# Kernel optimization log

Measured on AMD Instinct MI355X. Metric: run time of the kernel, lower is better.

Reference implementation:

```python
import jax, jax.numpy as jnp
import numpy as np

N_DISEASE, N_GENE, E, D = 20000, 100000, 2000000, 128


def setup_inputs() -> dict:
    key = jax.random.key(0)
    ks = jax.random.split(key, 12)
    s = 0.05  # weight scale keeps exp(logstd) well-behaved
    return {
        "x_disease": jax.random.normal(ks[0], (N_DISEASE, D), jnp.float32),
        "x_gene": jax.random.normal(ks[1], (N_GENE, D), jnp.float32),
        "edge_src": jax.random.randint(ks[2], (E,), 0, N_DISEASE, jnp.int32),
        "edge_dst": jax.random.randint(ks[3], (E,), 0, N_GENE, jnp.int32),
        "eps": jax.random.normal(ks[4], (N_GENE, D), jnp.float32),
        # SAGEConv (disease->gene): lin_l (on aggregated neighbors, with bias), lin_r (on dst root, no bias)
        "W_l": jax.random.normal(ks[5], (D, D), jnp.float32) * s,
        "b_l": jnp.zeros((D,), jnp.float32),
        "W_r": jax.random.normal(ks[6], (D, D), jnp.float32) * s,
        # fc_mu_gene / fc_logvar_gene
        "mu_W": jax.random.normal(ks[7], (D, D), jnp.float32) * s,
        "mu_b": jnp.zeros((D,), jnp.float32),
        "lv_W": jax.random.normal(ks[8], (D, D), jnp.float32) * s,
        "lv_b": jnp.zeros((D,), jnp.float32),
    }


def reference(x_disease, x_gene, edge_src, edge_dst, eps,
              W_l, b_l, W_r, mu_W, mu_b, lv_W, lv_b):
    # --- SAGEConv('disease' -> 'gene'), aggr='mean' ---
    msg = x_disease[edge_src]                                   # [E, D] gather
    summed = jax.ops.segment_sum(msg, edge_dst, num_segments=N_GENE)   # [N_gene, D]
    cnt = jax.ops.segment_sum(jnp.ones((msg.shape[0],), msg.dtype), edge_dst,
                              num_segments=N_GENE)
    mean = summed / jnp.maximum(cnt, 1.0)[:, None]
    h_gene = mean @ W_l + b_l + x_gene @ W_r                    # [N_gene, D]
    # (HeteroConv aggr='mean' is identity: only one relation targets 'gene')

    # --- mu / logstd heads + VGAE reparametrize ---
    mu = h_gene @ mu_W + mu_b
    logstd = h_gene @ lv_W + lv_b
    z = mu + eps * jnp.exp(logstd)
    return z
```

## Files before the change

### kernel.cpp

```cpp
#include <hip/hip_runtime.h>
#include <math.h>

#define D 128
#define ST 64
#define GBIN 256
#define CAP 6144
#define BCAP 8192
#define BK2_E 16
#define NBMAX 512

typedef short bf16x8 __attribute__((ext_vector_type(8)));
typedef short bf16x4 __attribute__((ext_vector_type(4)));
typedef float f32x4 __attribute__((ext_vector_type(4)));
typedef float f32x2 __attribute__((ext_vector_type(2)));

#if __has_builtin(__builtin_amdgcn_cvt_pk_f32_fp8) && __has_builtin(__builtin_amdgcn_cvt_pk_fp8_f32)
#define HW_FP8 1
#else
#define HW_FP8 0
#endif

__device__ inline unsigned short f2bf(float f) {
    union { float f; unsigned u; } v; v.f = f;
    unsigned r = v.u + 0x7fff + ((v.u >> 16) & 1);
    return (unsigned short)(r >> 16);
}
__device__ inline float bf2f(unsigned short u) {
    union { unsigned u; float f; } v; v.u = ((unsigned)u) << 16;
    return v.f;
}

__device__ inline unsigned f2fp8(float f) {
    union { float f; unsigned u; } v; v.f = f;
    unsigned s = v.u >> 31;
    unsigned mag = v.u & 0x7fffffffu;
    if (mag > 0x43E00000u) mag = 0x43E00000u;
    unsigned r = mag + 0x7FFFFu + ((mag >> 20) & 1);
    int e = (int)(r >> 23) - 120;
    unsigned out;
    if (e <= 0) {
        float ax;
        { union { unsigned u; float f; } w; w.u = mag; ax = w.f; }
        int m = (int)(ax * 512.0f + 0.5f);
        out = (m > 7) ? 8u : (unsigned)m;
    } else {
        out = ((unsigned)e << 3) | ((r >> 20) & 7);
    }
    return (s << 7) | out;
}
__device__ inline float fp8dec(unsigned b) {
    unsigned s = b >> 7, em = b & 0x7f;
    union { unsigned u; float f; } w;
    w.u = (em << 20) + 0x3C000000u;
    float v = (em >= 8) ? w.f : (float)(int)em * 0.001953125f;
    return s ? -v : v;
}

__device__ inline unsigned pack_fp8x4(float4 a) {
#if HW_FP8
    int r = __builtin_amdgcn_cvt_pk_fp8_f32(a.x, a.y, 0, false);
    r = __builtin_amdgcn_cvt_pk_fp8_f32(a.z, a.w, r, true);
    return (unsigned)r;
#else
    return f2fp8(a.x) | (f2fp8(a.y) << 8) | (f2fp8(a.z) << 16) | (f2fp8(a.w) << 24);
#endif
}
__device__ inline void unpack_fp8x4_add(unsigned w, f32x2* acc01, f32x2* acc23) {
#if HW_FP8
    f32x2 p0 = __builtin_amdgcn_cvt_pk_f32_fp8(w, false);
    f32x2 p1 = __builtin_amdgcn_cvt_pk_f32_fp8(w, true);
    *acc01 += p0;
    *acc23 += p1;
#else
    f32x2 p0 = { fp8dec(w & 0xff), fp8dec((w >> 8) & 0xff) };
    f32x2 p1 = { fp8dec((w >> 16) & 0xff), fp8dec((w >> 24) & 0xff) };
    *acc01 += p0;
    *acc23 += p1;
#endif
}

__global__ void init_bcur_kernel(int* __restrict__ bcur, int nbin)
{
    int b = blockIdx.x * blockDim.x + threadIdx.x;
    if (b < nbin) bcur[b] = b * BCAP;
}

__global__ __launch_bounds__(256) void bucket2_kernel(
    const int* __restrict__ esrc, const int* __restrict__ edst,
    int* __restrict__ bcur, unsigned* __restrict__ pairs2, int E, int nbin)
{
    __shared__ int lcount[NBMAX];
    __shared__ int lbase[NBMAX];
    int t = threadIdx.x;
    const int batch = 256 * BK2_E;
    for (long long base = (long long)blockIdx.x * batch; base < E;
         base += (long long)gridDim.x * batch) {
        for (int b = t; b < nbin; b += 256) lcount[b] = 0;
        __syncthreads();
        int bb[BK2_E], rr[BK2_E];
        unsigned pv[BK2_E];
        #pragma unroll
        for (int j = 0; j < BK2_E; ++j) {
            int e = (int)base + t + j * 256;
            bb[j] = -1;
            if (e < E) {
                int dd = __builtin_nontemporal_load(&edst[e]);
                int ss = __builtin_nontemporal_load(&esrc[e]);
                int bin = dd >> 8;
                bb[j] = bin;
                pv[j] = ((unsigned)(dd & (GBIN - 1)) << 16) | (unsigned)ss;
                rr[j] = atomicAdd(&lcount[bin], 1);
            }
        }
        __syncthreads();
        for (int b = t; b < nbin; b += 256)
            lbase[b] = lcount[b] ? atomicAdd(&bcur[b], lcount[b]) : 0;
        __syncthreads();
        #pragma unroll
        for (int j = 0; j < BK2_E; ++j)
            if (bb[j] >= 0) {
                int pos = lbase[bb[j]] + rr[j];
                if (pos < (bb[j] + 1) * BCAP)
                    pairs2[pos] = pv[j];
            }
        __syncthreads();
    }
}

__global__ __launch_bounds__(256) void fill3b_kernel(
    const unsigned* __restrict__ pairs2, const int* __restrict__ bcur,
    int* __restrict__ offs, int* __restrict__ oend,
    unsigned short* __restrict__ csr, int ngene)
{
    __shared__ int lhist[GBIN];
    __shared__ int lofs[GBIN];
    __shared__ int lcur[GBIN];
    __shared__ unsigned short stage[CAP];
    int b = blockIdx.x;
    int t = threadIdx.x;
    int g0 = b * GBIN;
    int ng = min(GBIN, ngene - g0);
    int sb = b * BCAP;
    int se = min(bcur[b], sb + BCAP);
    int n = se - sb;

    lhist[t] = 0;
    __syncthreads();
    for (int i = sb + t; i < se; i += 256)
        atomicAdd(&lhist[pairs2[i] >> 16], 1);
    __syncthreads();
    int v = lhist[t];
    lofs[t] = v;
    __syncthreads();
    for (int off = 1; off < GBIN; off <<= 1) {
        int add = (t >= off) ? lofs[t - off] : 0;
        __syncthreads();
        lofs[t] += add;
        __syncthreads();
    }
    int myofs = lofs[t] - v;
    lcur[t] = myofs;
    if (t < ng) {
        offs[g0 + t] = sb + myofs;
        oend[g0 + t] = sb + myofs + v;
    }
    __syncthreads();

    if (n <= CAP) {
        for (int i = sb + t; i < se; i += 256) {
            unsigned u = pairs2[i];
            int pos = atomicAdd(&lcur[u >> 16], 1);
            stage[pos] = (unsigned short)(u & 0xffffu);
        }
        __syncthreads();
        for (int i = t; i < n; i += 256)
            csr[sb + i] = stage[i];
    } else {
        for (int i = sb + t; i < se; i += 256) {
            unsigned u = pairs2[i];
            int pos = atomicAdd(&lcur[u >> 16], 1);
            csr[sb + pos] = (unsigned short)(u & 0xffffu);
        }
    }
}

__global__ __launch_bounds__(256) void cvt_kernel(
    const float* __restrict__ xd, unsigned char* __restrict__ xdb8, int nxd,
    const float* __restrict__ w0, const float* __restrict__ w1,
    const float* __restrict__ w2, const float* __restrict__ w3,
    unsigned short* __restrict__ t0, unsigned short* __restrict__ t1,
    unsigned short* __restrict__ t2, unsigned short* __restrict__ t3)
{
    int b = blockIdx.x;
    if (b < nxd) {
        int i = b * 256 + threadIdx.x;
        float4 a = ((const float4*)xd)[i * 2];
        float4 c = ((const float4*)xd)[i * 2 + 1];
        ((uint2*)xdb8)[i] = make_uint2(pack_fp8x4(a), pack_fp8x4(c));
    } else {
        int m = b - nxd;
        const float* src = m == 0 ? w0 : m == 1 ? w1 : m == 2 ? w2 : w3;
        unsigned short* dst = m == 0 ? t0 : m == 1 ? t1 : m == 2 ? t2 : t3;
        for (int idx = threadIdx.x; idx < D * D; idx += 256) {
            int k = idx >> 7, n = idx & 127;
            dst[n * D + k] = f2bf(src[idx]);
        }
    }
}

__global__ __launch_bounds__(256, 6) void gather_kernel(
    const int* __restrict__ offs, const int* __restrict__ oend,
    const unsigned short* __restrict__ csr,
    const unsigned char* __restrict__ xdb8, unsigned short* __restrict__ meanb,
    int ngene)
{
    int tid = threadIdx.x;
    int r = tid >> 4, c = tid & 15;
    int row = blockIdx.x * 16 + r;
    if (row >= ngene) return;
    int beg = offs[row], end = oend[row];
    const uint2* tab = (const uint2*)xdb8;
    f32x2 a0[4] = {{0,0},{0,0},{0,0},{0,0}};
    f32x2 a1[4] = {{0,0},{0,0},{0,0},{0,0}};
    int i = beg;
    for (; i + 2 <= end; i += 2) {
        int s0 = csr[i], s1 = csr[i + 1];
        uint2 v0 = tab[s0 * 16 + c];
        uint2 v1 = tab[s1 * 16 + c];
        unpack_fp8x4_add(v0.x, &a0[0], &a0[1]);
        unpack_fp8x4_add(v0.y, &a0[2], &a0[3]);
        unpack_fp8x4_add(v1.x, &a1[0], &a1[1]);
        unpack_fp8x4_add(v1.y, &a1[2], &a1[3]);
    }
    if (i < end) {
        int s0 = csr[i];
        uint2 v0 = tab[s0 * 16 + c];
        unpack_fp8x4_add(v0.x, &a0[0], &a0[1]);
        unpack_fp8x4_add(v0.y, &a0[2], &a0[3]);
    }
    float inv = 1.0f / fmaxf((float)(end - beg), 1.0f);
    bf16x8 o;
    #pragma unroll
    for (int j = 0; j < 4; ++j) {
        f32x2 s = a0[j] + a1[j];
        o[j * 2]     = (short)f2bf(s[0] * inv);
        o[j * 2 + 1] = (short)f2bf(s[1] * inv);
    }
    ((bf16x8*)meanb)[row * 16 + c] = o;
}

__global__ __launch_bounds__(512, 4) void hz_kernel(
    const unsigned short* __restrict__ meanb, const float* __restrict__ xg,
    const float* __restrict__ eps,
    const unsigned short* __restrict__ WlT, const unsigned short* __restrict__ WrT,
    const unsigned short* __restrict__ muT, const unsigned short* __restrict__ lvT,
    const float* __restrict__ bl, const float* __restrict__ mub,
    const float* __restrict__ lvb, float* __restrict__ z, int ngene, int nst)
{
    __shared__ unsigned short mean_s[ST][132];
    __shared__ unsigned short xg_s[ST][132];
    __shared__ unsigned short h_s[ST][132];

    int tid = threadIdx.x;
    int wave = tid >> 6;
    int lane = tid & 63;
    int lr = lane & 15;
    int lg = lane >> 4;
    int cb = wave * 16;
    int nb = cb + lg * 4;

    float4 bl4 = *(const float4*)&bl[nb];
    float4 mb4 = *(const float4*)&mub[nb];
    float4 lb4 = *(const float4*)&lvb[nb];

    for (int st = blockIdx.x; st < nst; st += gridDim.x) {
        int rowbase = st * ST;

        f32x4 epr[4];
        #pragma unroll
        for (int rt = 0; rt < 4; ++rt) {
            int orow = rowbase + rt * 16 + lr;
            if (orow >= ngene) orow = ngene - 1;
            epr[rt] = *(const f32x4*)&eps[(size_t)orow * D + nb];
        }

        for (int i = tid; i < ST * 16; i += 512) {
            int row = i >> 4, c = i & 15;
            int grow = rowbase + row;
            if (grow >= ngene) grow = ngene - 1;
            *(bf16x8*)&mean_s[row][c * 8] =
                *(const bf16x8*)&meanb[(size_t)grow * D + c * 8];
            const float* xp = &xg[(size_t)grow * D + c * 8];
            float4 x0 = *(const float4*)xp;
            float4 x1 = *(const float4*)(xp + 4);
            bf16x8 v;
            v[0] = (short)f2bf(x0.x); v[1] = (short)f2bf(x0.y);
            v[2] = (short)f2bf(x0.z); v[3] = (short)f2bf(x0.w);
            v[4] = (short)f2bf(x1.x); v[5] = (short)f2bf(x1.y);
            v[6] = (short)f2bf(x1.z); v[7] = (short)f2bf(x1.w);
            *(bf16x8*)&xg_s[row][c * 8] = v;
        }
        __syncthreads();

        {
            bf16x8 wl[4], wr[4];
            #pragma unroll
            for (int kc = 0; kc < 4; ++kc) {
                int koff = kc * 32 + lg * 8;
                wl[kc] = *(const bf16x8*)&WlT[(cb + lr) * D + koff];
                wr[kc] = *(const bf16x8*)&WrT[(cb + lr) * D + koff];
            }
            #pragma unroll
            for (int rt = 0; rt < 4; ++rt) {
                int r0 = rt * 16 + lr;
                f32x4 accm = {bl4.x, bl4.y, bl4.z, bl4.w};
                f32x4 accx = {0.f, 0.f, 0.f, 0.f};
                #pragma unroll
                for (int kc = 0; kc < 4; ++kc) {
                    int koff = kc * 32 + lg * 8;
                    bf16x8 am = *(const bf16x8*)&mean_s[r0][koff];
                    bf16x8 ax = *(const bf16x8*)&xg_s[r0][koff];
                    accm = __builtin_amdgcn_mfma_f32_16x16x32_bf16(wl[kc], am, accm, 0, 0, 0);
                    accx = __builtin_amdgcn_mfma_f32_16x16x32_bf16(wr[kc], ax, accx, 0, 0, 0);
                }
                bf16x4 hp;
                #pragma unroll
                for (int r = 0; r < 4; ++r) hp[r] = (short)f2bf(accm[r] + accx[r]);
                *(bf16x4*)&h_s[r0][nb] = hp;
            }
        }
        __syncthreads();

        {
            bf16x8 mu[4], lv[4];
            #pragma unroll
            for (int kc = 0; kc < 4; ++kc) {
                int koff = kc * 32 + lg * 8;
                mu[kc] = *(const bf16x8*)&muT[(cb + lr) * D + koff];
                lv[kc] = *(const bf16x8*)&lvT[(cb + lr) * D + koff];
            }
            #pragma unroll
            for (int rt = 0; rt < 4; ++rt) {
                int r0 = rt * 16 + lr;
                f32x4 zm = {mb4.x, mb4.y, mb4.z, mb4.w};
                f32x4 zl = {lb4.x, lb4.y, lb4.z, lb4.w};
                #pragma unroll
                for (int kc = 0; kc < 4; ++kc) {
                    int koff = kc * 32 + lg * 8;
                    bf16x8 ah = *(const bf16x8*)&h_s[r0][koff];
                    zm = __builtin_amdgcn_mfma_f32_16x16x32_bf16(mu[kc], ah, zm, 0, 0, 0);
                    zl = __builtin_amdgcn_mfma_f32_16x16x32_bf16(lv[kc], ah, zl, 0, 0, 0);
                }
                int orow = rowbase + r0;
                if (orow < ngene) {
                    float4 zo;
                    zo.x = zm[0] + epr[rt][0] * __expf(zl[0]);
                    zo.y = zm[1] + epr[rt][1] * __expf(zl[1]);
                    zo.z = zm[2] + epr[rt][2] * __expf(zl[2]);
                    zo.w = zm[3] + epr[rt][3] * __expf(zl[3]);
                    *(float4*)&z[(size_t)orow * D + nb] = zo;
                }
            }
        }
        __syncthreads();
    }
}

extern "C" void kernel_launch(void* const* d_in, const int* in_sizes, int n_in,
                              void* d_out, int out_size, void* d_ws, size_t ws_size,
                              hipStream_t stream)
{
    const float* xd  = (const float*)d_in[0];
    const float* xg  = (const float*)d_in[1];
    const int* esrc  = (const int*)d_in[2];
    const int* edst  = (const int*)d_in[3];
    const float* eps = (const float*)d_in[4];
    const float* Wl  = (const float*)d_in[5];
    const float* bl  = (const float*)d_in[6];
    const float* Wr  = (const float*)d_in[7];
    const float* muW = (const float*)d_in[8];
    const float* mub = (const float*)d_in[9];
    const float* lvW = (const float*)d_in[10];
    const float* lvb = (const float*)d_in[11];

    int E = in_sizes[2];
    int ndis = in_sizes[0] / D;
    int ngene = in_sizes[1] / D;
    int nbin = (ngene + GBIN - 1) / GBIN;

    char* p = (char*)d_ws;
    int* offs = (int*)p;  p += (size_t)ngene * 4;
    int* oend = (int*)p;  p += (size_t)ngene * 4;
    int* bcur = (int*)p;  p += NBMAX * 4;
    p = (char*)(((size_t)p + 255) & ~(size_t)255);
    unsigned char* xdb8 = (unsigned char*)p;  p += (size_t)ndis * D;
    unsigned short* WlT = (unsigned short*)p; p += D * D * 2;
    unsigned short* WrT = (unsigned short*)p; p += D * D * 2;
    unsigned short* muT = (unsigned short*)p; p += D * D * 2;
    unsigned short* lvT = (unsigned short*)p; p += D * D * 2;
    p = (char*)(((size_t)p + 255) & ~(size_t)255);
    unsigned* pairs2 = (unsigned*)p;          p += (size_t)nbin * BCAP * 4;
    unsigned short* csr_src = (unsigned short*)p; p += (size_t)nbin * BCAP * 2;
    p = (char*)(((size_t)p + 255) & ~(size_t)255);
    unsigned short* meanb = (unsigned short*)p;

    init_bcur_kernel<<<(nbin + 255) / 256, 256, 0, stream>>>(bcur, nbin);
    bucket2_kernel<<<512, 256, 0, stream>>>(esrc, edst, bcur, pairs2, E, nbin);
    fill3b_kernel<<<nbin, 256, 0, stream>>>(pairs2, bcur, offs, oend, csr_src, ngene);

    int nxd = ndis * D / 8 / 256;
    cvt_kernel<<<nxd + 4, 256, 0, stream>>>(xd, xdb8, nxd,
                                            Wl, Wr, muW, lvW, WlT, WrT, muT, lvT);

    gather_kernel<<<(ngene + 15) / 16, 256, 0, stream>>>(offs, oend, csr_src,
                                                         xdb8, meanb, ngene);

    int nst = (ngene + ST - 1) / ST;
    hz_kernel<<<512, 512, 0, stream>>>(meanb, xg, eps, WlT, WrT, muT, lvT,
                                       bl, mub, lvb, (float*)d_out, ngene, nst);
}
```

Before: 144.9 us.

## Register-prefetch next tile of mean and x_gene in hz_kernel, raise grid size

The hz_kernel now loads the next row tile's mean and x_gene values into registers right after the shared-memory barrier. The global load latency can then overlap with the MFMA work on the current tile instead of stalling at the start of each iteration. The grid also grows from 512 to 768 blocks. The prefetch buffers add registers per thread, which may reduce occupancy. With nst around 1563 tiles, the larger grid changes how many loop iterations each block runs.

Result: slower. 178.5 us (+23.2%).

```diff
diff --git a/kernel.cpp b/kernel.cpp
--- a/kernel.cpp
+++ b/kernel.cpp
@@ -269,9 +269,29 @@
     int cb = wave * 16;
     int nb = cb + lg * 4;
 
+    int row0 = tid >> 4, c0 = tid & 15;
+    int row1 = row0 + 32;
+
     float4 bl4 = *(const float4*)&bl[nb];
     float4 mb4 = *(const float4*)&mub[nb];
     float4 lb4 = *(const float4*)&lvb[nb];
+
+    bf16x8 pm0, pm1;
+    f32x4 px00, px01, px10, px11;
+
+    auto load_tile = [&](int st) {
+        int rb = st * ST;
+        int g0 = rb + row0; if (g0 >= ngene) g0 = ngene - 1;
+        int g1 = rb + row1; if (g1 >= ngene) g1 = ngene - 1;
+        pm0 = *(const bf16x8*)&meanb[(size_t)g0 * D + c0 * 8];
+        pm1 = *(const bf16x8*)&meanb[(size_t)g1 * D + c0 * 8];
+        const f32x4* xp0 = (const f32x4*)&xg[(size_t)g0 * D + c0 * 8];
+        const f32x4* xp1 = (const f32x4*)&xg[(size_t)g1 * D + c0 * 8];
+        px00 = xp0[0]; px01 = xp0[1];
+        px10 = xp1[0]; px11 = xp1[1];
+    };
+
+    if (blockIdx.x < nst) load_tile(blockIdx.x);
 
     for (int st = blockIdx.x; st < nst; st += gridDim.x) {
         int rowbase = st * ST;
@@ -284,23 +304,25 @@
             epr[rt] = *(const f32x4*)&eps[(size_t)orow * D + nb];
         }
 
-        for (int i = tid; i < ST * 16; i += 512) {
-            int row = i >> 4, c = i & 15;
-            int grow = rowbase + row;
-            if (grow >= ngene) grow = ngene - 1;
-            *(bf16x8*)&mean_s[row][c * 8] =
-                *(const bf16x8*)&meanb[(size_t)grow * D + c * 8];
-            const float* xp = &xg[(size_t)grow * D + c * 8];
-            float4 x0 = *(const float4*)xp;
-            float4 x1 = *(const float4*)(xp + 4);
+        {
+            *(bf16x8*)&mean_s[row0][c0 * 8] = pm0;
+            *(bf16x8*)&mean_s[row1][c0 * 8] = pm1;
             bf16x8 v;
-            v[0] = (short)f2bf(x0.x); v[1] = (short)f2bf(x0.y);
-            v[2] = (short)f2bf(x0.z); v[3] = (short)f2bf(x0.w);
-            v[4] = (short)f2bf(x1.x); v[5] = (short)f2bf(x1.y);
-            v[6] = (short)f2bf(x1.z); v[7] = (short)f2bf(x1.w);
-            *(bf16x8*)&xg_s[row][c * 8] = v;
-        }
-        __syncthreads();
+            v[0] = (short)f2bf(px00[0]); v[1] = (short)f2bf(px00[1]);
+            v[2] = (short)f2bf(px00[2]); v[3] = (short)f2bf(px00[3]);
+            v[4] = (short)f2bf(px01[0]); v[5] = (short)f2bf(px01[1]);
+            v[6] = (short)f2bf(px01[2]); v[7] = (short)f2bf(px01[3]);
+            *(bf16x8*)&xg_s[row0][c0 * 8] = v;
+            v[0] = (short)f2bf(px10[0]); v[1] = (short)f2bf(px10[1]);
+            v[2] = (short)f2bf(px10[2]); v[3] = (short)f2bf(px10[3]);
+            v[4] = (short)f2bf(px11[0]); v[5] = (short)f2bf(px11[1]);
+            v[6] = (short)f2bf(px11[2]); v[7] = (short)f2bf(px11[3]);
+            *(bf16x8*)&xg_s[row1][c0 * 8] = v;
+        }
+        __syncthreads();
+
+        int stn = st + gridDim.x;
+        if (stn < nst) load_tile(stn);
 
         {
             bf16x8 wl[4], wr[4];
@@ -416,6 +438,6 @@
                                                          xdb8, meanb, ngene);
 
     int nst = (ngene + ST - 1) / ST;
-    hz_kernel<<<512, 512, 0, stream>>>(meanb, xg, eps, WlT, WrT, muT, lvT,
+    hz_kernel<<<768, 512, 0, stream>>>(meanb, xg, eps, WlT, WrT, muT, lvT,
                                        bl, mub, lvb, (float*)d_out, ngene, nst);
 }
```
